# Kernel optimization log

Hardware: AMD Instinct MI355X
Metric: run time of the kernel (lower is better)

The kernel has to match this reference:

```python
import jax, jax.numpy as jnp
import numpy as np

BN_EPS = 1e-5


def setup_inputs() -> dict:
    key = jax.random.key(0)
    k1, k2, k3 = jax.random.split(key, 3)
    N, C_IN, C_OUT, K = 200000, 32, 64, 27
    data_in = jax.random.normal(k1, (1, C_IN, N, 1), dtype=jnp.float32)
    # Octree neighbor table: for each octant, indices of its 27 (3x3x3) neighbors.
    # ocnn uses -1 for empty neighbors; indices here are all valid, but the
    # reference still masks negatives for faithfulness.
    neigh = jax.random.randint(k2, (N, K), 0, N, dtype=jnp.int64)
    weight = jax.random.normal(k3, (C_OUT, C_IN, K), dtype=jnp.float32) * 0.05
    bn_gamma = jnp.ones((C_OUT,), dtype=jnp.float32)
    bn_beta = jnp.zeros((C_OUT,), dtype=jnp.float32)
    return {"data_in": data_in, "neigh": neigh, "weight": weight,
            "bn_gamma": bn_gamma, "bn_beta": bn_beta}


def reference(data_in, neigh, weight, bn_gamma, bn_beta):
    # data_in: [1, C_in, N, 1] (ocnn octree feature layout)
    x = data_in[0, :, :, 0]                      # [C_in, N]
    valid = neigh >= 0                           # [N, 27]
    idx = jnp.where(valid, neigh, 0)
    # octree2col: gather 27 neighbor features per octant -> [C_in, N, 27]
    col = x[:, idx] * valid[None, :, :].astype(x.dtype)
    # grouped GEMM: weight [C_out, C_in, 27] contracted with col
    out = jnp.einsum('ock,cnk->on', weight, col)  # [C_out, N]
    # BatchNorm2d in training mode: batch stats over the node axis, biased var
    mean = jnp.mean(out, axis=1, keepdims=True)
    var = jnp.mean(jnp.square(out - mean), axis=1, keepdims=True)
    out = (out - mean) * jax.lax.rsqrt(var + BN_EPS)
    out = out * bn_gamma[:, None] + bn_beta[:, None]
    out = jax.nn.relu(out)
    return out[None, :, :, None]                 # [1, C_out, N, 1]
```

## Files before the change

kernel.cpp:

```cpp
#include <hip/hip_runtime.h>

#define N_PTS 200000
#define C_IN  32
#define C_OUT 64
#define K_NB  27
#define BN_EPS 1e-5f

using bf16x8 = __attribute__((ext_vector_type(8))) short;
using f32x4  = __attribute__((ext_vector_type(4))) float;

#define M_WT_OFF  0
#define M_AB_OFF  114688
#define M_PS_OFF  115200
#define M_XT_OFF  131072
#define M_NT_OFF  (131072 + 12800064)
#define M_WS_NEED ((size_t)M_NT_OFF + 29ull * N_PTS * 4ull)

#define F_WTK_OFF 0
#define F_AB_OFF  221184
#define F_Z_OFF   221696
#define F_PS_OFF  221824

__device__ __forceinline__ unsigned short f2bf(float f) {
    unsigned int u = __float_as_uint(f);
    u = (u + 0x7fffu + ((u >> 16) & 1u)) >> 16;
    return (unsigned short)u;
}

__global__ void k_prep_x(const float* __restrict__ x, unsigned short* __restrict__ xt) {
    int n = blockIdx.x * 256 + threadIdx.x;
    if (n > N_PTS) return;
    unsigned short row[C_IN];
    if (n == N_PTS) {
#pragma unroll
        for (int c = 0; c < C_IN; ++c) row[c] = 0;
    } else {
#pragma unroll
        for (int c = 0; c < C_IN; ++c) row[c] = f2bf(x[(long long)c * N_PTS + n]);
    }
    uint4* dst = (uint4*)(xt + (long long)n * C_IN);
#pragma unroll
    for (int q = 0; q < 4; ++q) dst[q] = ((const uint4*)row)[q];
}

__global__ void k_prep_w(const float* __restrict__ w, unsigned short* __restrict__ wt) {
    int i = blockIdx.x * 256 + threadIdx.x;
    if (i >= 28 * C_OUT * C_IN) return;
    int c = i & 31, o = (i >> 5) & 63, k = i >> 11;
    wt[i] = (k < K_NB) ? f2bf(w[(o * C_IN + c) * K_NB + k]) : (unsigned short)0;
}

__global__ void k_prep_n(const int* __restrict__ neigh, int* __restrict__ nt) {
    int n = blockIdx.x * 256 + threadIdx.x;
    if (n >= N_PTS) return;
    int v[K_NB];
#pragma unroll
    for (int k = 0; k < K_NB; ++k) v[k] = neigh[n * K_NB + k];
#pragma unroll
    for (int k = 0; k < K_NB; ++k) {
        int t = v[k];
        nt[(long long)k * N_PTS + n] = (t >= 0 && t < N_PTS) ? t : N_PTS;
    }
    nt[27ll * N_PTS + n] = N_PTS;
    nt[28ll * N_PTS + n] = N_PTS;
}

__launch_bounds__(256, 3)
__global__ void k_conv_mfma(const unsigned short* __restrict__ xt,
                            const int* __restrict__ nt,
                            const unsigned short* __restrict__ wt,
                            float* __restrict__ out) {
    const int lane = threadIdx.x & 63;
    const int wv   = threadIdx.x >> 6;
    const int n0   = blockIdx.x * 256 + wv * 64;
    if (n0 >= N_PTS) return;
    const int l15 = lane & 15, lq = lane >> 4;

    const unsigned short* xt_q = xt + lq * 8;
    const unsigned short* wt_q = wt + l15 * C_IN + lq * 8;
    const int nbase = n0 + l15;

    f32x4 acc[4][4];
#pragma unroll
    for (int g = 0; g < 4; ++g)
#pragma unroll
        for (int ot = 0; ot < 4; ++ot) acc[g][ot] = f32x4{0.f, 0.f, 0.f, 0.f};

    int tb[4];
    bf16x8 bc[4], ac[4];
    {
        int t0[4];
#pragma unroll
        for (int g = 0; g < 4; ++g) t0[g] = nt[nbase + 16 * g];
#pragma unroll
        for (int g = 0; g < 4; ++g) tb[g] = nt[N_PTS + nbase + 16 * g];
#pragma unroll
        for (int g = 0; g < 4; ++g) bc[g] = *(const bf16x8*)(xt_q + (long long)t0[g] * C_IN);
#pragma unroll
        for (int ot = 0; ot < 4; ++ot) ac[ot] = *(const bf16x8*)(wt_q + ot * 512);
    }

    for (int k = 0; k < K_NB; ++k) {
        int tn[4];
#pragma unroll
        for (int g = 0; g < 4; ++g) tn[g] = nt[(long long)(k + 2) * N_PTS + nbase + 16 * g];
        bf16x8 an[4];
#pragma unroll
        for (int ot = 0; ot < 4; ++ot) an[ot] = *(const bf16x8*)(wt_q + (k + 1) * 2048 + ot * 512);
        bf16x8 bn[4];
#pragma unroll
        for (int g = 0; g < 4; ++g) bn[g] = *(const bf16x8*)(xt_q + (long long)tb[g] * C_IN);

#pragma unroll
        for (int g = 0; g < 4; ++g)
#pragma unroll
            for (int ot = 0; ot < 4; ++ot)
                acc[g][ot] = __builtin_amdgcn_mfma_f32_16x16x32_bf16(ac[ot], bc[g], acc[g][ot], 0, 0, 0);

#pragma unroll
        for (int g = 0; g < 4; ++g) { bc[g] = bn[g]; tb[g] = tn[g]; }
#pragma unroll
        for (int ot = 0; ot < 4; ++ot) ac[ot] = an[ot];
    }

#pragma unroll
    for (int ot = 0; ot < 4; ++ot)
#pragma unroll
        for (int r = 0; r < 4; ++r) {
            float* o = out + (long long)(ot * 16 + lq * 4 + r) * N_PTS + n0 + l15;
#pragma unroll
            for (int g = 0; g < 4; ++g) o[16 * g] = acc[g][ot][r];
        }
}

__global__ void k_wt_f32(const float* __restrict__ w, float* __restrict__ wtk) {
    int i = blockIdx.x * 256 + threadIdx.x;
    if (i >= K_NB * C_IN * C_OUT) return;
    int o = i & 63, r = i >> 6, c = r & 31, k = r >> 5;
    wtk[i] = w[(o * C_IN + c) * K_NB + k];
}

__launch_bounds__(256, 1)
__global__ void k_conv_f32(const float* __restrict__ src, const int* __restrict__ neigh,
                           const float* __restrict__ wtk, float* __restrict__ out) {
    __shared__ float wt_s[C_IN * C_OUT];
    const int lane = threadIdx.x & 63;
    const int wave = threadIdx.x >> 6;
    const int n0   = blockIdx.x * 64 + wave * 16;
    float acc[16];
#pragma unroll
    for (int p = 0; p < 16; ++p) acc[p] = 0.f;
    for (int k = 0; k < K_NB; ++k) {
        __syncthreads();
#pragma unroll
        for (int j = 0; j < 8; ++j)
            wt_s[threadIdx.x + j * 256] = wtk[k * (C_IN * C_OUT) + threadIdx.x + j * 256];
        __syncthreads();
        int t[16];
#pragma unroll
        for (int p = 0; p < 16; ++p) t[p] = neigh[(n0 + p) * K_NB + k];
#pragma unroll
        for (int c = 0; c < C_IN; ++c) {
            float wv = wt_s[c * C_OUT + lane];
#pragma unroll
            for (int p = 0; p < 16; ++p) {
                float xv = (t[p] >= 0) ? src[(long long)c * N_PTS + t[p]] : 0.f;
                acc[p] = fmaf(wv, xv, acc[p]);
            }
        }
    }
    float4* dst = (float4*)(out + (long long)lane * N_PTS + n0);
#pragma unroll
    for (int q = 0; q < 4; ++q) dst[q] = ((const float4*)acc)[q];
}

__global__ void k_stats1(const float* __restrict__ raw, float* __restrict__ ps) {
    int o = blockIdx.x & 63, sl = blockIdx.x >> 6;
    const int per = N_PTS / 8;
    const float4* row = (const float4*)(raw + (long long)o * N_PTS + (long long)sl * per);
    float s = 0.f, s2 = 0.f;
    for (int i = threadIdx.x; i < per / 4; i += 256) {
        float4 v = row[i];
        s  += v.x + v.y + v.z + v.w;
        s2 += v.x * v.x + v.y * v.y + v.z * v.z + v.w * v.w;
    }
#pragma unroll
    for (int off = 32; off > 0; off >>= 1) {
        s  += __shfl_down(s, off, 64);
        s2 += __shfl_down(s2, off, 64);
    }
    __shared__ float r0[4], r1[4];
    int wv = threadIdx.x >> 6;
    if ((threadIdx.x & 63) == 0) { r0[wv] = s; r1[wv] = s2; }
    __syncthreads();
    if (threadIdx.x == 0) {
        ps[blockIdx.x]       = r0[0] + r0[1] + r0[2] + r0[3];
        ps[512 + blockIdx.x] = r1[0] + r1[1] + r1[2] + r1[3];
    }
}

__global__ void k_stats2(const float* __restrict__ ps, const float* __restrict__ gamma,
                         const float* __restrict__ beta, float* __restrict__ ab) {
    int o = threadIdx.x;
    float S = 0.f, S2 = 0.f;
#pragma unroll
    for (int sl = 0; sl < 8; ++sl) {
        S  += ps[sl * 64 + o];
        S2 += ps[512 + sl * 64 + o];
    }
    float mean = S / (float)N_PTS;
    float var  = S2 / (float)N_PTS - mean * mean;
    float a = gamma[o] * rsqrtf(var + BN_EPS);
    float b = beta[o] - mean * a;
    ab[o]      = a;
    ab[64 + o] = b;
}

__global__ void k_norm(float* __restrict__ out, const float* __restrict__ ab) {
    int i = blockIdx.x * 256 + threadIdx.x;
    const int total4 = (C_OUT * N_PTS) / 4;
    if (i >= total4) return;
    int o = (i * 4) / N_PTS;
    float a = ab[o], b = ab[64 + o];
    float4 v = ((float4*)out)[i];
    v.x = fmaxf(fmaf(v.x, a, b), 0.f);
    v.y = fmaxf(fmaf(v.y, a, b), 0.f);
    v.z = fmaxf(fmaf(v.z, a, b), 0.f);
    v.w = fmaxf(fmaf(v.w, a, b), 0.f);
    ((float4*)out)[i] = v;
}

extern "C" void kernel_launch(void* const* d_in, const int* in_sizes, int n_in,
                              void* d_out, int out_size, void* d_ws, size_t ws_size,
                              hipStream_t stream) {
    const float* x   = (const float*)d_in[0];
    const int*   nb  = (const int*)d_in[1];
    const float* w   = (const float*)d_in[2];
    const float* gam = (const float*)d_in[3];
    const float* bet = (const float*)d_in[4];
    float* out = (float*)d_out;
    char* ws = (char*)d_ws;

    if (ws_size >= M_WS_NEED) {
        unsigned short* wt = (unsigned short*)(ws + M_WT_OFF);
        float*          ab = (float*)(ws + M_AB_OFF);
        float*          ps = (float*)(ws + M_PS_OFF);
        unsigned short* xt = (unsigned short*)(ws + M_XT_OFF);
        int*            nt = (int*)(ws + M_NT_OFF);

        k_prep_x<<<(N_PTS + 256) / 256, 256, 0, stream>>>(x, xt);
        k_prep_w<<<(28 * C_OUT * C_IN + 255) / 256, 256, 0, stream>>>(w, wt);
        k_prep_n<<<(N_PTS + 255) / 256, 256, 0, stream>>>(nb, nt);
        k_conv_mfma<<<(N_PTS + 255) / 256, 256, 0, stream>>>(xt, nt, wt, out);
        k_stats1<<<512, 256, 0, stream>>>(out, ps);
        k_stats2<<<1, 64, 0, stream>>>(ps, gam, bet, ab);
        k_norm<<<((C_OUT * N_PTS) / 4 + 255) / 256, 256, 0, stream>>>(out, ab);
    } else {
        float* wtk  = (float*)(ws + F_WTK_OFF);
        float* ab   = (float*)(ws + F_AB_OFF);
        float* zbuf = (float*)(ws + F_Z_OFF);
        float* ps   = (float*)(ws + F_PS_OFF);
        hipMemsetAsync(zbuf, 0, C_IN * sizeof(float), stream);
        k_wt_f32<<<(K_NB * C_IN * C_OUT + 255) / 256, 256, 0, stream>>>(w, wtk);
        k_conv_f32<<<N_PTS / 64, 256, 0, stream>>>(x, nb, wtk, out);
        k_stats1<<<512, 256, 0, stream>>>(out, ps);
        k_stats2<<<1, 64, 0, stream>>>(ps, gam, bet, ab);
        k_norm<<<((C_OUT * N_PTS) / 4 + 255) / 256, 256, 0, stream>>>(out, ab);
    }
}
```

Baseline: 147.1 us.

## Fuse BN statistics into MFMA conv epilogue and merge prep kernels

The conv kernel now computes per-block channel sums and sums of squares with shuffles and shared memory, writing partials that a per-channel reduction kernel turns into scale and shift. This removes the separate stats pass that re-read the full output. The x and neighbour prep kernels are merged into one, and the conv is restructured to 16 points per wave with a 3-deep gather prefetch and higher occupancy (launch bounds 6), replacing the 64-point-per-wave register tiling. The trade-off is more blocks, each reloading weights per k, and less register reuse of the A operands.

Measured after the change: 163.5 us. 11.1% more time.

```diff
diff --git a/kernel.cpp b/kernel.cpp
--- a/kernel.cpp
+++ b/kernel.cpp
@@ -5,6 +5,7 @@
 #define C_OUT 64
 #define K_NB  27
 #define BN_EPS 1e-5f
+#define NBLK  3125
 
 using bf16x8 = __attribute__((ext_vector_type(8))) short;
 using f32x4  = __attribute__((ext_vector_type(4))) float;
@@ -12,9 +13,9 @@
 #define M_WT_OFF  0
 #define M_AB_OFF  114688
 #define M_PS_OFF  115200
-#define M_XT_OFF  131072
-#define M_NT_OFF  (131072 + 12800064)
-#define M_WS_NEED ((size_t)M_NT_OFF + 29ull * N_PTS * 4ull)
+#define M_XT_OFF  1835008
+#define M_NT_OFF  (1835008 + 12800064)
+#define M_WS_NEED ((size_t)M_NT_OFF + 27ull * N_PTS * 4ull)
 
 #define F_WTK_OFF 0
 #define F_AB_OFF  221184
@@ -25,22 +26,6 @@
     unsigned int u = __float_as_uint(f);
     u = (u + 0x7fffu + ((u >> 16) & 1u)) >> 16;
     return (unsigned short)u;
-}
-
-__global__ void k_prep_x(const float* __restrict__ x, unsigned short* __restrict__ xt) {
-    int n = blockIdx.x * 256 + threadIdx.x;
-    if (n > N_PTS) return;
-    unsigned short row[C_IN];
-    if (n == N_PTS) {
-#pragma unroll
-        for (int c = 0; c < C_IN; ++c) row[c] = 0;
-    } else {
-#pragma unroll
-        for (int c = 0; c < C_IN; ++c) row[c] = f2bf(x[(long long)c * N_PTS + n]);
-    }
-    uint4* dst = (uint4*)(xt + (long long)n * C_IN);
-#pragma unroll
-    for (int q = 0; q < 4; ++q) dst[q] = ((const uint4*)row)[q];
 }
 
 __global__ void k_prep_w(const float* __restrict__ w, unsigned short* __restrict__ wt) {
@@ -50,139 +35,119 @@
     wt[i] = (k < K_NB) ? f2bf(w[(o * C_IN + c) * K_NB + k]) : (unsigned short)0;
 }
 
-__global__ void k_prep_n(const int* __restrict__ neigh, int* __restrict__ nt) {
+__global__ void k_prep_xn(const float* __restrict__ x, const int* __restrict__ neigh,
+                          unsigned short* __restrict__ xt, int* __restrict__ nt) {
     int n = blockIdx.x * 256 + threadIdx.x;
-    if (n >= N_PTS) return;
-    int v[K_NB];
-#pragma unroll
-    for (int k = 0; k < K_NB; ++k) v[k] = neigh[n * K_NB + k];
-#pragma unroll
-    for (int k = 0; k < K_NB; ++k) {
-        int t = v[k];
-        nt[(long long)k * N_PTS + n] = (t >= 0 && t < N_PTS) ? t : N_PTS;
-    }
-    nt[27ll * N_PTS + n] = N_PTS;
-    nt[28ll * N_PTS + n] = N_PTS;
-}
-
-__launch_bounds__(256, 3)
+    if (n > N_PTS) return;
+    unsigned short row[C_IN];
+    if (n == N_PTS) {
+#pragma unroll
+        for (int c = 0; c < C_IN; ++c) row[c] = 0;
+    } else {
+#pragma unroll
+        for (int c = 0; c < C_IN; ++c) row[c] = f2bf(x[(long long)c * N_PTS + n]);
+    }
+    uint4* dst = (uint4*)(xt + (long long)n * C_IN);
+#pragma unroll
+    for (int q = 0; q < 4; ++q) dst[q] = ((const uint4*)row)[q];
+
+    if (n < N_PTS) {
+#pragma unroll
+        for (int k = 0; k < K_NB; ++k) {
+            int t = neigh[n * K_NB + k];
+            nt[k * N_PTS + n] = (t >= 0 && t < N_PTS) ? t : N_PTS;
+        }
+    }
+}
+
+__launch_bounds__(256, 6)
 __global__ void k_conv_mfma(const unsigned short* __restrict__ xt,
                             const int* __restrict__ nt,
                             const unsigned short* __restrict__ wt,
-                            float* __restrict__ out) {
+                            float* __restrict__ out,
+                            float* __restrict__ ps) {
+    __shared__ float sred[512];
     const int lane = threadIdx.x & 63;
     const int wv   = threadIdx.x >> 6;
-    const int n0   = blockIdx.x * 256 + wv * 64;
-    if (n0 >= N_PTS) return;
-    const int l15 = lane & 15, lq = lane >> 4;
+    const int n0   = blockIdx.x * 64 + wv * 16;
+    const int l15  = lane & 15, lq = lane >> 4;
 
     const unsigned short* xt_q = xt + lq * 8;
     const unsigned short* wt_q = wt + l15 * C_IN + lq * 8;
-    const int nbase = n0 + l15;
-
-    f32x4 acc[4][4];
-#pragma unroll
-    for (int g = 0; g < 4; ++g)
-#pragma unroll
-        for (int ot = 0; ot < 4; ++ot) acc[g][ot] = f32x4{0.f, 0.f, 0.f, 0.f};
-
-    int tb[4];
-    bf16x8 bc[4], ac[4];
+    const int nb = n0 + l15;
+
+    f32x4 acc[4];
+#pragma unroll
+    for (int ot = 0; ot < 4; ++ot) acc[ot] = f32x4{0.f, 0.f, 0.f, 0.f};
+
+    int t2;
+    bf16x8 B0, B1;
     {
-        int t0[4];
-#pragma unroll
-        for (int g = 0; g < 4; ++g) t0[g] = nt[nbase + 16 * g];
-#pragma unroll
-        for (int g = 0; g < 4; ++g) tb[g] = nt[N_PTS + nbase + 16 * g];
-#pragma unroll
-        for (int g = 0; g < 4; ++g) bc[g] = *(const bf16x8*)(xt_q + (long long)t0[g] * C_IN);
-#pragma unroll
-        for (int ot = 0; ot < 4; ++ot) ac[ot] = *(const bf16x8*)(wt_q + ot * 512);
+        int t0 = nt[nb];
+        int t1 = nt[N_PTS + nb];
+        t2     = nt[2 * N_PTS + nb];
+        B0 = *(const bf16x8*)(xt_q + (long long)t0 * C_IN);
+        B1 = *(const bf16x8*)(xt_q + (long long)t1 * C_IN);
     }
 
     for (int k = 0; k < K_NB; ++k) {
-        int tn[4];
-#pragma unroll
-        for (int g = 0; g < 4; ++g) tn[g] = nt[(long long)(k + 2) * N_PTS + nbase + 16 * g];
-        bf16x8 an[4];
-#pragma unroll
-        for (int ot = 0; ot < 4; ++ot) an[ot] = *(const bf16x8*)(wt_q + (k + 1) * 2048 + ot * 512);
-        bf16x8 bn[4];
-#pragma unroll
-        for (int g = 0; g < 4; ++g) bn[g] = *(const bf16x8*)(xt_q + (long long)tb[g] * C_IN);
-
-#pragma unroll
-        for (int g = 0; g < 4; ++g)
-#pragma unroll
-            for (int ot = 0; ot < 4; ++ot)
-                acc[g][ot] = __builtin_amdgcn_mfma_f32_16x16x32_bf16(ac[ot], bc[g], acc[g][ot], 0, 0, 0);
-
-#pragma unroll
-        for (int g = 0; g < 4; ++g) { bc[g] = bn[g]; tb[g] = tn[g]; }
-#pragma unroll
-        for (int ot = 0; ot < 4; ++ot) ac[ot] = an[ot];
+        bf16x8 B2 = *(const bf16x8*)(xt_q + (long long)t2 * C_IN);
+        int krow = k + 3; if (krow > K_NB - 1) krow = K_NB - 1;
+        int t3 = nt[krow * N_PTS + nb];
+        bf16x8 A[4];
+#pragma unroll
+        for (int ot = 0; ot < 4; ++ot)
+            A[ot] = *(const bf16x8*)(wt_q + k * 2048 + ot * 512);
+#pragma unroll
+        for (int ot = 0; ot < 4; ++ot)
+            acc[ot] = __builtin_amdgcn_mfma_f32_16x16x32_bf16(A[ot], B0, acc[ot], 0, 0, 0);
+        B0 = B1; B1 = B2; t2 = t3;
     }
 
 #pragma unroll
     for (int ot = 0; ot < 4; ++ot)
 #pragma unroll
-        for (int r = 0; r < 4; ++r) {
-            float* o = out + (long long)(ot * 16 + lq * 4 + r) * N_PTS + n0 + l15;
-#pragma unroll
-            for (int g = 0; g < 4; ++g) o[16 * g] = acc[g][ot][r];
-        }
-}
-
-__global__ void k_wt_f32(const float* __restrict__ w, float* __restrict__ wtk) {
-    int i = blockIdx.x * 256 + threadIdx.x;
-    if (i >= K_NB * C_IN * C_OUT) return;
-    int o = i & 63, r = i >> 6, c = r & 31, k = r >> 5;
-    wtk[i] = w[(o * C_IN + c) * K_NB + k];
-}
-
-__launch_bounds__(256, 1)
-__global__ void k_conv_f32(const float* __restrict__ src, const int* __restrict__ neigh,
-                           const float* __restrict__ wtk, float* __restrict__ out) {
-    __shared__ float wt_s[C_IN * C_OUT];
-    const int lane = threadIdx.x & 63;
-    const int wave = threadIdx.x >> 6;
-    const int n0   = blockIdx.x * 64 + wave * 16;
-    float acc[16];
-#pragma unroll
-    for (int p = 0; p < 16; ++p) acc[p] = 0.f;
-    for (int k = 0; k < K_NB; ++k) {
-        __syncthreads();
-#pragma unroll
-        for (int j = 0; j < 8; ++j)
-            wt_s[threadIdx.x + j * 256] = wtk[k * (C_IN * C_OUT) + threadIdx.x + j * 256];
-        __syncthreads();
-        int t[16];
-#pragma unroll
-        for (int p = 0; p < 16; ++p) t[p] = neigh[(n0 + p) * K_NB + k];
-#pragma unroll
-        for (int c = 0; c < C_IN; ++c) {
-            float wv = wt_s[c * C_OUT + lane];
-#pragma unroll
-            for (int p = 0; p < 16; ++p) {
-                float xv = (t[p] >= 0) ? src[(long long)c * N_PTS + t[p]] : 0.f;
-                acc[p] = fmaf(wv, xv, acc[p]);
+        for (int r = 0; r < 4; ++r)
+            out[(ot * 16 + lq * 4 + r) * N_PTS + nb] = acc[ot][r];
+
+    f32x4 sq[4];
+#pragma unroll
+    for (int ot = 0; ot < 4; ++ot) sq[ot] = acc[ot] * acc[ot];
+#pragma unroll
+    for (int d = 1; d < 16; d <<= 1) {
+#pragma unroll
+        for (int ot = 0; ot < 4; ++ot)
+#pragma unroll
+            for (int r = 0; r < 4; ++r) {
+                acc[ot][r] += __shfl_xor(acc[ot][r], d);
+                sq[ot][r]  += __shfl_xor(sq[ot][r], d);
             }
-        }
-    }
-    float4* dst = (float4*)(out + (long long)lane * N_PTS + n0);
-#pragma unroll
-    for (int q = 0; q < 4; ++q) dst[q] = ((const float4*)acc)[q];
-}
-
-__global__ void k_stats1(const float* __restrict__ raw, float* __restrict__ ps) {
-    int o = blockIdx.x & 63, sl = blockIdx.x >> 6;
-    const int per = N_PTS / 8;
-    const float4* row = (const float4*)(raw + (long long)o * N_PTS + (long long)sl * per);
+    }
+    if (l15 == 0) {
+#pragma unroll
+        for (int ot = 0; ot < 4; ++ot)
+#pragma unroll
+            for (int r = 0; r < 4; ++r) {
+                int ch = ot * 16 + lq * 4 + r;
+                sred[wv * 128 + ch]      = acc[ot][r];
+                sred[wv * 128 + 64 + ch] = sq[ot][r];
+            }
+    }
+    __syncthreads();
+    if (threadIdx.x < 128) {
+        float v = sred[threadIdx.x] + sred[128 + threadIdx.x] +
+                  sred[256 + threadIdx.x] + sred[384 + threadIdx.x];
+        ps[blockIdx.x * 128 + threadIdx.x] = v;
+    }
+}
+
+__global__ void k_stats2(const float* __restrict__ ps, const float* __restrict__ gamma,
+                         const float* __restrict__ beta, float* __restrict__ ab) {
+    int ch = blockIdx.x;
     float s = 0.f, s2 = 0.f;
-    for (int i = threadIdx.x; i < per / 4; i += 256) {
-        float4 v = row[i];
-        s  += v.x + v.y + v.z + v.w;
-        s2 += v.x * v.x + v.y * v.y + v.z * v.z + v.w * v.w;
+    for (int b = threadIdx.x; b < NBLK; b += 256) {
+        s  += ps[b * 128 + ch];
+        s2 += ps[b * 128 + 64 + ch];
     }
 #pragma unroll
     for (int off = 32; off > 0; off >>= 1) {
@@ -194,26 +159,15 @@
     if ((threadIdx.x & 63) == 0) { r0[wv] = s; r1[wv] = s2; }
     __syncthreads();
     if (threadIdx.x == 0) {
-        ps[blockIdx.x]       = r0[0] + r0[1] + r0[2] + r0[3];
-        ps[512 + blockIdx.x] = r1[0] + r1[1] + r1[2] + r1[3];
-    }
-}
-
-__global__ void k_stats2(const float* __restrict__ ps, const float* __restrict__ gamma,
-                         const float* __restrict__ beta, float* __restrict__ ab) {
-    int o = threadIdx.x;
-    float S = 0.f, S2 = 0.f;
-#pragma unroll
-    for (int sl = 0; sl < 8; ++sl) {
-        S  += ps[sl * 64 + o];
-        S2 += ps[512 + sl * 64 + o];
-    }
-    float mean = S / (float)N_PTS;
-    float var  = S2 / (float)N_PTS - mean * mean;
-    float a = gamma[o] * rsqrtf(var + BN_EPS);
-    float b = beta[o] - mean * a;
-    ab[o]      = a;
-    ab[64 + o] = b;
+        float S = r0[0] + r0[1] + r0[2] + r0[3];
+        float S2 = r1[0] + r1[1] + r1[2] + r1[3];
+        float mean = S / (float)N_PTS;
+        float var  = S2 / (float)N_PTS - mean * mean;
+        float a = gamma[ch] * rsqrtf(var + BN_EPS);
+        float b = beta[ch] - mean * a;
+        ab[ch]      = a;
+        ab[64 + ch] = b;
+    }
 }
 
 __global__ void k_norm(float* __restrict__ out, const float* __restrict__ ab) {
@@ -230,6 +184,89 @@
     ((float4*)out)[i] = v;
 }
 
+__global__ void k_wt_f32(const float* __restrict__ w, float* __restrict__ wtk) {
+    int i = blockIdx.x * 256 + threadIdx.x;
+    if (i >= K_NB * C_IN * C_OUT) return;
+    int o = i & 63, r = i >> 6, c = r & 31, k = r >> 5;
+    wtk[i] = w[(o * C_IN + c) * K_NB + k];
+}
+
+__launch_bounds__(256, 1)
+__global__ void k_conv_f32(const float* __restrict__ src, const int* __restrict__ neigh,
+                           const float* __restrict__ wtk, float* __restrict__ out) {
+    __shared__ float wt_s[C_IN * C_OUT];
+    const int lane = threadIdx.x & 63;
+    const int wave = threadIdx.x >> 6;
+    const int n0   = blockIdx.x * 64 + wave * 16;
+    float acc[16];
+#pragma unroll
+    for (int p = 0; p < 16; ++p) acc[p] = 0.f;
+    for (int k = 0; k < K_NB; ++k) {
+        __syncthreads();
+#pragma unroll
+        for (int j = 0; j < 8; ++j)
+            wt_s[threadIdx.x + j * 256] = wtk[k * (C_IN * C_OUT) + threadIdx.x + j * 256];
+        __syncthreads();
+        int t[16];
+#pragma unroll
+        for (int p = 0; p < 16; ++p) t[p] = neigh[(n0 + p) * K_NB + k];
+#pragma unroll
+        for (int c = 0; c < C_IN; ++c) {
+            float wv = wt_s[c * C_OUT + lane];
+#pragma unroll
+            for (int p = 0; p < 16; ++p) {
+                float xv = (t[p] >= 0) ? src[(long long)c * N_PTS + t[p]] : 0.f;
+                acc[p] = fmaf(wv, xv, acc[p]);
+            }
+        }
+    }
+    float4* dst = (float4*)(out + (long long)lane * N_PTS + n0);
+#pragma unroll
+    for (int q = 0; q < 4; ++q) dst[q] = ((const float4*)acc)[q];
+}
+
+__global__ void k_stats1(const float* __restrict__ raw, float* __restrict__ ps) {
+    int o = blockIdx.x & 63, sl = blockIdx.x >> 6;
+    const int per = N_PTS / 8;
+    const float4* row = (const float4*)(raw + (long long)o * N_PTS + (long long)sl * per);
+    float s = 0.f, s2 = 0.f;
+    for (int i = threadIdx.x; i < per / 4; i += 256) {
+        float4 v = row[i];
+        s  += v.x + v.y + v.z + v.w;
+        s2 += v.x * v.x + v.y * v.y + v.z * v.z + v.w * v.w;
+    }
+#pragma unroll
+    for (int off = 32; off > 0; off >>= 1) {
+        s  += __shfl_down(s, off, 64);
+        s2 += __shfl_down(s2, off, 64);
+    }
+    __shared__ float r0[4], r1[4];
+    int wv = threadIdx.x >> 6;
+    if ((threadIdx.x & 63) == 0) { r0[wv] = s; r1[wv] = s2; }
+    __syncthreads();
+    if (threadIdx.x == 0) {
+        ps[blockIdx.x]       = r0[0] + r0[1] + r0[2] + r0[3];
+        ps[512 + blockIdx.x] = r1[0] + r1[1] + r1[2] + r1[3];
+    }
+}
+
+__global__ void k_stats2f(const float* __restrict__ ps, const float* __restrict__ gamma,
+                          const float* __restrict__ beta, float* __restrict__ ab) {
+    int o = threadIdx.x;
+    float S = 0.f, S2 = 0.f;
+#pragma unroll
+    for (int sl = 0; sl < 8; ++sl) {
+        S  += ps[sl * 64 + o];
+        S2 += ps[512 + sl * 64 + o];
+    }
+    float mean = S / (float)N_PTS;
+    float var  = S2 / (float)N_PTS - mean * mean;
+    float a = gamma[o] * rsqrtf(var + BN_EPS);
+    float b = beta[o] - mean * a;
+    ab[o]      = a;
+    ab[64 + o] = b;
+}
+
 extern "C" void kernel_launch(void* const* d_in, const int* in_sizes, int n_in,
                               void* d_out, int out_size, void* d_ws, size_t ws_size,
                               hipStream_t stream) {
@@ -248,23 +285,19 @@
         unsigned short* xt = (unsigned short*)(ws + M_XT_OFF);
         int*            nt = (int*)(ws + M_NT_OFF);
 
-        k_prep_x<<<(N_PTS + 256) / 256, 256, 0, stream>>>(x, xt);
         k_prep_w<<<(28 * C_OUT * C_IN + 255) / 256, 256, 0, stream>>>(w, wt);
-        k_prep_n<<<(N_PTS + 255) / 256, 256, 0, stream>>>(nb, nt);
-        k_conv_mfma<<<(N_PTS + 255) / 256, 256, 0, stream>>>(xt, nt, wt, out);
-        k_stats1<<<512, 256, 0, stream>>>(out, ps);
-        k_stats2<<<1, 64, 0, stream>>>(ps, gam, bet, ab);
+        k_prep_xn<<<(N_PTS + 256) / 256, 256, 0, stream>>>(x, nb, xt, nt);
+        k_conv_mfma<<<NBLK, 256, 0, stream>>>(xt, nt, wt, out, ps);
+        k_stats2<<<C_OUT, 256, 0, stream>>>(ps, gam, bet, ab);
         k_norm<<<((C_OUT * N_PTS) / 4 + 255) / 256, 256, 0, stream>>>(out, ab);
     } else {
         float* wtk  = (float*)(ws + F_WTK_OFF);
         float* ab   = (float*)(ws + F_AB_OFF);
-        float* zbuf = (float*)(ws + F_Z_OFF);
         float* ps   = (float*)(ws + F_PS_OFF);
-        hipMemsetAsync(zbuf, 0, C_IN * sizeof(float), stream);
         k_wt_f32<<<(K_NB * C_IN * C_OUT + 255) / 256, 256, 0, stream>>>(w, wtk);
         k_conv_f32<<<N_PTS / 64, 256, 0, stream>>>(x, nb, wtk, out);
         k_stats1<<<512, 256, 0, stream>>>(out, ps);
-        k_stats2<<<1, 64, 0, stream>>>(ps, gam, bet, ab);
+        k_stats2f<<<1, 64, 0, stream>>>(ps, gam, bet, ab);
         k_norm<<<((C_OUT * N_PTS) / 4 + 255) / 256, 256, 0, stream>>>(out, ab);
     }
 }
```
